# Optimization experiments

Hardware: AMD Instinct MI355X
Metric: run time of the kernel (lower is better)

## Reference

```python
import jax, jax.numpy as jnp
import numpy as np

N_NODES = 50000
D = 128
N_EDGES = 800000


def _gcn_layer(h, W, b, row, col, mask, n_nodes):
    # Linear: h @ W.T + b  (nn.Linear convention)
    h = h @ W.T + b
    # degree of source nodes, counting only non-self-loop edges (remove_self_loops)
    deg = jax.ops.segment_sum(mask.astype(h.dtype), row, num_segments=n_nodes)
    deg_inv_sqrt = jnp.where(deg > 0, jax.lax.rsqrt(jnp.maximum(deg, 1.0)), 0.0)
    norm = deg_inv_sqrt[row] * deg_inv_sqrt[col] * mask.astype(h.dtype)
    # gather-scale messages [E, D], scatter-add into target nodes (col)
    msg = norm[:, None] * h[row]
    return jax.ops.segment_sum(msg, col, num_segments=n_nodes)


def setup_inputs() -> dict:
    key = jax.random.key(0)
    ks = jax.random.split(key, 9)
    x = jax.random.normal(ks[0], (N_NODES, D), dtype=jnp.float32)
    edge_index = jax.random.randint(ks[1], (2, N_EDGES), 0, N_NODES, dtype=jnp.int64)
    lim = 1.0 / np.sqrt(D)
    params = {}
    for i in range(3):
        params[f"W{i}"] = jax.random.uniform(ks[2 + 2 * i], (D, D), jnp.float32, -lim, lim)
        params[f"b{i}"] = jax.random.uniform(ks[3 + 2 * i], (D,), jnp.float32, -lim, lim)
    return {"x": x, "edge_index": edge_index, **params}


def reference(x, edge_index, W0, b0, W1, b1, W2, b2):
    row, col = edge_index[0], edge_index[1]
    mask = row != col  # remove_self_loops
    h = x
    for W, b in ((W0, b0), (W1, b1), (W2, b2)):
        h_new = jax.nn.relu(_gcn_layer(h, W, b, row, col, mask, x.shape[0]))
        h = h + h_new
    return h
```

## Files before the change

### kernel.cpp

```cpp
#include <hip/hip_runtime.h>
#include <hip/hip_bf16.h>


#define D_DIM 128
#define SCAN_CHUNK 1024
#define CHUNKS 64
#define LDSW 12512

typedef __attribute__((ext_vector_type(8))) short bf16x8;
typedef __attribute__((ext_vector_type(4))) float f32x4;

static __device__ __forceinline__ short f2bf(float f) {
    union { __hip_bfloat16 b; short s; } u;
    u.b = __float2bfloat16(f);
    return u.s;
}
static __device__ __forceinline__ float bf_lo(unsigned p) { return __uint_as_float(p << 16); }
static __device__ __forceinline__ float bf_hi(unsigned p) { return __uint_as_float(p & 0xffff0000u); }


__global__ __launch_bounds__(256) void hist_kernel(const int* __restrict__ ei,
                                                   unsigned* __restrict__ partial_col,
                                                   unsigned* __restrict__ partial_row,
                                                   int E, int CHSZ) {
    __shared__ unsigned hh[LDSW];
    int tid = threadIdx.x;
    int ch = blockIdx.x;
    int docol = (blockIdx.y == 0);
    for (int i = tid; i < LDSW; i += 256) hh[i] = 0u;
    __syncthreads();
    int e0 = ch * CHSZ, e1 = min(e0 + CHSZ, E);
    for (int e = e0 + tid; e < e1; e += 256) {
        int row = ei[e];
        int col = ei[E + e];
        if (row == col) continue;
        int bin = docol ? col : row;
        atomicAdd(&hh[bin >> 2], 1u << ((bin & 3) * 8));
    }
    __syncthreads();
    unsigned* dst = (docol ? partial_col : partial_row) + ch * LDSW;
    for (int i = tid; i < LDSW; i += 256) dst[i] = hh[i];
}

__global__ __launch_bounds__(256) void reduce_scan_kernel(
    const unsigned* __restrict__ partial_col, const unsigned* __restrict__ partial_row,
    int* __restrict__ col_cnt, float* __restrict__ dis, int* __restrict__ bsum,
    int NW ) {
    __shared__ int wsum[4];
    int w = blockIdx.x * 256 + threadIdx.x;
    int s = 0;
    if (w < NW) {
        unsigned clo = 0, chi = 0, rlo = 0, rhi = 0;
#pragma unroll 4
        for (int ch = 0; ch < CHUNKS; ch++) {
            unsigned wc = partial_col[ch * LDSW + w];
            unsigned wr = partial_row[ch * LDSW + w];
            clo += wc & 0x00FF00FFu; chi += (wc >> 8) & 0x00FF00FFu;
            rlo += wr & 0x00FF00FFu; rhi += (wr >> 8) & 0x00FF00FFu;
        }
        int c0 = clo & 0xFFFF, c1 = chi & 0xFFFF, c2 = clo >> 16, c3 = chi >> 16;
        int r0 = rlo & 0xFFFF, r1 = rhi & 0xFFFF, r2 = rlo >> 16, r3 = rhi >> 16;
        ((int4*)col_cnt)[w] = make_int4(c0, c1, c2, c3);
        float4 dv;
        dv.x = (r0 > 0) ? rsqrtf((float)r0) : 0.0f;
        dv.y = (r1 > 0) ? rsqrtf((float)r1) : 0.0f;
        dv.z = (r2 > 0) ? rsqrtf((float)r2) : 0.0f;
        dv.w = (r3 > 0) ? rsqrtf((float)r3) : 0.0f;
        ((float4*)dis)[w] = dv;
        s = c0 + c1 + c2 + c3;
    }
#pragma unroll
    for (int d = 32; d > 0; d >>= 1) s += __shfl_down(s, d, 64);
    int lane = threadIdx.x & 63, wv = threadIdx.x >> 6;
    if (lane == 0) wsum[wv] = s;
    __syncthreads();
    if (threadIdx.x == 0) bsum[blockIdx.x] = wsum[0] + wsum[1] + wsum[2] + wsum[3];
}

__global__ __launch_bounds__(64) void scan_bbase_kernel(const int* __restrict__ bsum,
                                                        int* __restrict__ bbase,
                                                        int* __restrict__ offs,
                                                        int G, int n) {
    int lane = threadIdx.x;
    int v = (lane < G) ? bsum[lane] : 0;
    int s = v;
#pragma unroll
    for (int d = 1; d < 64; d <<= 1) {
        int t = __shfl_up(s, d, 64);
        if (lane >= d) s += t;
    }
    if (lane < G) bbase[lane] = s - v;
    if (lane == 63) offs[n] = s;
}

__global__ __launch_bounds__(256) void scan_final_kernel(const int* __restrict__ cnt,
                                                         const int* __restrict__ bbase,
                                                         int* __restrict__ offs, int n) {
    __shared__ int wsum[4];
    int base = blockIdx.x * SCAN_CHUNK;
    int tid = threadIdx.x;
    const int PT = SCAN_CHUNK / 256;
    int v[PT];
    int s = 0;
#pragma unroll
    for (int i = 0; i < PT; i++) {
        int g = base + tid * PT + i;
        v[i] = (g < n) ? cnt[g] : 0;
        s += v[i];
    }
    int local_sum = s;
    int lane = tid & 63, w = tid >> 6;
#pragma unroll
    for (int d = 1; d < 64; d <<= 1) {
        int t = __shfl_up(s, d, 64);
        if (lane >= d) s += t;
    }
    if (lane == 63) wsum[w] = s;
    __syncthreads();
    int wbase = 0;
    for (int i = 0; i < w; i++) wbase += wsum[i];
    int run = bbase[blockIdx.x] + wbase + (s - local_sum);
#pragma unroll
    for (int i = 0; i < PT; i++) {
        int g = base + tid * PT + i;
        if (g < n) offs[g] = run;
        run += v[i];
    }
}

__global__ __launch_bounds__(256) void base_kernel(const unsigned* __restrict__ partial_col,
                                                   const int* __restrict__ offs,
                                                   int* __restrict__ base,
                                                   int N, int NW) {
    int w = blockIdx.x * 256 + threadIdx.x;
    if (w >= NW) return;
    int4 run = ((const int4*)offs)[w];
    for (int ch = 0; ch < CHUNKS; ch++) {
        unsigned wd = partial_col[ch * LDSW + w];
        ((int4*)(base + ch * N))[w] = run;
        run.x += (int)(wd & 0xFF);
        run.y += (int)((wd >> 8) & 0xFF);
        run.z += (int)((wd >> 16) & 0xFF);
        run.w += (int)(wd >> 24);
    }
}

__global__ __launch_bounds__(256) void scatter_kernel(const int* __restrict__ ei,
                                                      const float* __restrict__ dis,
                                                      const int* __restrict__ base,
                                                      int2* __restrict__ epack,
                                                      int E, int N, int CHSZ) {
    __shared__ unsigned cur[LDSW];
    int tid = threadIdx.x;
    int ch = blockIdx.x;
    for (int i = tid; i < LDSW; i += 256) cur[i] = 0u;
    __syncthreads();
    int e0 = ch * CHSZ, e1 = min(e0 + CHSZ, E);
    const int* bch = base + ch * N;
    for (int e = e0 + tid; e < e1; e += 256) {
        int row = ei[e];
        int col = ei[E + e];
        if (row == col) continue;
        float w = dis[row] * dis[col];
        int sh = (col & 3) * 8;
        unsigned old = atomicAdd(&cur[col >> 2], 1u << sh);
        int slot = bch[col] + (int)((old >> sh) & 0xFF);
        epack[slot] = make_int2(row * (D_DIM / 2), __float_as_int(w));
    }
}

__global__ void wcvt_all_kernel(const float* __restrict__ W0, const float* __restrict__ W1,
                                const float* __restrict__ W2, unsigned short* __restrict__ B0,
                                unsigned short* __restrict__ B1, unsigned short* __restrict__ B2) {
    int i = blockIdx.x * blockDim.x + threadIdx.x;
    const float* W = (blockIdx.y == 0) ? W0 : (blockIdx.y == 1) ? W1 : W2;
    unsigned short* B = (blockIdx.y == 0) ? B0 : (blockIdx.y == 1) ? B1 : B2;
    if (i < D_DIM * D_DIM) B[i] = (unsigned short)f2bf(W[i]);
}


__global__ __launch_bounds__(256) void linear_mfma_kernel(
    const float* __restrict__ A, const unsigned short* __restrict__ Wb,
    const float* __restrict__ bias, unsigned short* __restrict__ hWb, int nrows) {
    int wave = threadIdx.x >> 6;
    int lane = threadIdx.x & 63;
    int r0 = blockIdx.x * 64 + wave * 16;
    int m = lane & 15, q = lane >> 4;
    int rload = min(r0 + m, nrows - 1);
    const float4* h4 = (const float4*)A;

    f32x4 acc[8];
#pragma unroll
    for (int jt = 0; jt < 8; jt++) acc[jt] = (f32x4){0.f, 0.f, 0.f, 0.f};

#pragma unroll
    for (int k0 = 0; k0 < 128; k0 += 32) {
        int c0 = k0 + q * 8;
        float4 x0 = h4[rload * 32 + (c0 >> 2)];
        float4 x1 = h4[rload * 32 + (c0 >> 2) + 1];
        bf16x8 a;
        a[0] = f2bf(x0.x); a[1] = f2bf(x0.y); a[2] = f2bf(x0.z); a[3] = f2bf(x0.w);
        a[4] = f2bf(x1.x); a[5] = f2bf(x1.y); a[6] = f2bf(x1.z); a[7] = f2bf(x1.w);
#pragma unroll
        for (int jt = 0; jt < 8; jt++) {
            bf16x8 b = *(const bf16x8*)(Wb + (jt * 16 + m) * D_DIM + c0);
            acc[jt] = __builtin_amdgcn_mfma_f32_16x16x32_bf16(a, b, acc[jt], 0, 0, 0);
        }
    }

#pragma unroll
    for (int jt = 0; jt < 8; jt++) {
        int col = jt * 16 + m;
        float bv = bias[col];
#pragma unroll
        for (int reg = 0; reg < 4; reg++) {
            int rr = r0 + q * 4 + reg;
            if (rr < nrows) hWb[(size_t)rr * D_DIM + col] = (unsigned short)f2bf(acc[jt][reg] + bv);
        }
    }
}

__global__ __launch_bounds__(256) void agg_kernel(const int* __restrict__ offs,
                                                  const int2* __restrict__ epack,
                                                  const unsigned int* __restrict__ hW2,
                                                  const float* __restrict__ hprev,
                                                  float* __restrict__ hout, int n_nodes) {
    int node = (int)((blockIdx.x * blockDim.x + threadIdx.x) >> 6);
    int lane = threadIdx.x & 63;
    if (node >= n_nodes) return;

    int beg = offs[node];
    int end = offs[node + 1];

    float ax8[8], ay8[8];
#pragma unroll
    for (int u = 0; u < 8; u++) { ax8[u] = 0.f; ay8[u] = 0.f; }

    int i = beg;
    for (; i + 8 <= end; i += 8) {
        int2 e[8];
        unsigned p[8];
#pragma unroll
        for (int u = 0; u < 8; u++) e[u] = epack[i + u];
#pragma unroll
        for (int u = 0; u < 8; u++) p[u] = hW2[e[u].x + lane];
#pragma unroll
        for (int u = 0; u < 8; u++) {
            float w = __int_as_float(e[u].y);
            ax8[u] = fmaf(w, bf_lo(p[u]), ax8[u]);
            ay8[u] = fmaf(w, bf_hi(p[u]), ay8[u]);
        }
    }
    int rem = end - i;
    if (rem & 4) {
        int2 e[4];
        unsigned p[4];
#pragma unroll
        for (int u = 0; u < 4; u++) e[u] = epack[i + u];
#pragma unroll
        for (int u = 0; u < 4; u++) p[u] = hW2[e[u].x + lane];
#pragma unroll
        for (int u = 0; u < 4; u++) {
            float w = __int_as_float(e[u].y);
            ax8[u] = fmaf(w, bf_lo(p[u]), ax8[u]);
            ay8[u] = fmaf(w, bf_hi(p[u]), ay8[u]);
        }
        i += 4;
    }
    if (rem & 2) {
        int2 e0 = epack[i], e1 = epack[i + 1];
        unsigned p0 = hW2[e0.x + lane], p1 = hW2[e1.x + lane];
        float w0 = __int_as_float(e0.y), w1 = __int_as_float(e1.y);
        ax8[4] = fmaf(w0, bf_lo(p0), ax8[4]); ay8[4] = fmaf(w0, bf_hi(p0), ay8[4]);
        ax8[5] = fmaf(w1, bf_lo(p1), ax8[5]); ay8[5] = fmaf(w1, bf_hi(p1), ay8[5]);
        i += 2;
    }
    if (rem & 1) {
        int2 e0 = epack[i];
        unsigned p0 = hW2[e0.x + lane];
        float w0 = __int_as_float(e0.y);
        ax8[6] = fmaf(w0, bf_lo(p0), ax8[6]); ay8[6] = fmaf(w0, bf_hi(p0), ay8[6]);
    }
    float ax = ((ax8[0] + ax8[1]) + (ax8[2] + ax8[3])) + ((ax8[4] + ax8[5]) + (ax8[6] + ax8[7]));
    float ay = ((ay8[0] + ay8[1]) + (ay8[2] + ay8[3])) + ((ay8[4] + ay8[5]) + (ay8[6] + ay8[7]));

    int idx = node * (D_DIM / 2) + lane;
    float2 hv = ((const float2*)hprev)[idx];
    float2 o;
    o.x = hv.x + fmaxf(ax, 0.0f);
    o.y = hv.y + fmaxf(ay, 0.0f);
    ((float2*)hout)[idx] = o;
}


static inline size_t align_up(size_t x, size_t a) { return (x + a - 1) & ~(a - 1); }

extern "C" void kernel_launch(void* const* d_in, const int* in_sizes, int n_in,
                              void* d_out, int out_size, void* d_ws, size_t ws_size,
                              hipStream_t stream) {
    const float* x = (const float*)d_in[0];
    const int* ei = (const int*)d_in[1];
    const float* Wl[3] = {(const float*)d_in[2], (const float*)d_in[4], (const float*)d_in[6]};
    const float* bl[3] = {(const float*)d_in[3], (const float*)d_in[5], (const float*)d_in[7]};

    const int N = in_sizes[0] / D_DIM;
    const int E = in_sizes[1] / 2;
    const int NW = N / 4;
    const int G = (N + SCAN_CHUNK - 1) / SCAN_CHUNK;
    const int CHSZ = (E + CHUNKS - 1) / CHUNKS;

    char* p = (char*)d_ws;
    int* col_cnt = (int*)p;            p += align_up((size_t)N * 4, 256);
    int* offs    = (int*)p;            p += align_up((size_t)(N + 1) * 4, 256);
    float* dis   = (float*)p;          p += align_up((size_t)N * 4, 256);
    int* bsum    = (int*)p;            p += align_up((size_t)64 * 4, 256);
    int* bbase   = (int*)p;            p += align_up((size_t)64 * 4, 256);
    unsigned* partial_col = (unsigned*)p;  p += align_up((size_t)CHUNKS * LDSW * 4, 256);
    unsigned* partial_row = (unsigned*)p;  p += align_up((size_t)CHUNKS * LDSW * 4, 256);
    int* base    = (int*)p;            p += align_up((size_t)CHUNKS * N * 4, 256);
    unsigned short* Wb[3];
    for (int l = 0; l < 3; l++) { Wb[l] = (unsigned short*)p; p += align_up((size_t)D_DIM * D_DIM * 2, 256); }
    int2* epack  = (int2*)p;           p += align_up((size_t)E * 8, 256);
    unsigned short* hWb = (unsigned short*)p;  p += align_up((size_t)N * D_DIM * 2, 256);
    (void)ws_size;

    hist_kernel<<<dim3(CHUNKS, 2), 256, 0, stream>>>(ei, partial_col, partial_row, E, CHSZ);
    reduce_scan_kernel<<<(NW + 255) / 256, 256, 0, stream>>>(partial_col, partial_row,
                                                             col_cnt, dis, bsum, NW);
    scan_bbase_kernel<<<1, 64, 0, stream>>>(bsum, bbase, offs, G, N);
    scan_final_kernel<<<G, 256, 0, stream>>>(col_cnt, bbase, offs, N);
    base_kernel<<<(NW + 255) / 256, 256, 0, stream>>>(partial_col, offs, base, N, NW);
    scatter_kernel<<<CHUNKS, 256, 0, stream>>>(ei, dis, base, epack, E, N, CHSZ);
    wcvt_all_kernel<<<dim3((D_DIM * D_DIM + 255) / 256, 3), 256, 0, stream>>>(
        Wl[0], Wl[1], Wl[2], Wb[0], Wb[1], Wb[2]);

    const float* hprev = x;
    float* h = (float*)d_out;
    int gemm_blocks = (N + 63) / 64;
    int agg_blocks = (N + 3) / 4;
    for (int l = 0; l < 3; l++) {
        linear_mfma_kernel<<<gemm_blocks, 256, 0, stream>>>(hprev, Wb[l], bl[l], hWb, N);
        agg_kernel<<<agg_blocks, 256, 0, stream>>>(offs, epack, (const unsigned int*)hWb, hprev, h, N);
        hprev = h;
    }
}
```

Baseline: 363.5 us.

## Quadruple edge chunks and replace per-chunk base array with grouped byte prefixes

```diff
diff --git a/kernel.cpp b/kernel.cpp
--- a/kernel.cpp
+++ b/kernel.cpp
@@ -4,7 +4,9 @@
 
 #define D_DIM 128
 #define SCAN_CHUNK 1024
-#define CHUNKS 64
+#define CHUNKS 256
+#define GROUPS 8
+#define GS (CHUNKS / GROUPS)
 #define LDSW 12512
 
 typedef __attribute__((ext_vector_type(8))) short bf16x8;
@@ -38,23 +40,46 @@
         atomicAdd(&hh[bin >> 2], 1u << ((bin & 3) * 8));
     }
     __syncthreads();
-    unsigned* dst = (docol ? partial_col : partial_row) + ch * LDSW;
+    unsigned* dst = (docol ? partial_col : partial_row) + (size_t)ch * LDSW;
     for (int i = tid; i < LDSW; i += 256) dst[i] = hh[i];
 }
 
-__global__ __launch_bounds__(256) void reduce_scan_kernel(
-    const unsigned* __restrict__ partial_col, const unsigned* __restrict__ partial_row,
-    int* __restrict__ col_cnt, float* __restrict__ dis, int* __restrict__ bsum,
-    int NW ) {
+__global__ __launch_bounds__(256) void group_prefix_kernel(
+    unsigned* __restrict__ partial_col, const unsigned* __restrict__ partial_row,
+    unsigned* __restrict__ gsum_col, unsigned* __restrict__ gsum_row, int NW) {
+    int w = blockIdx.x * 256 + threadIdx.x;
+    if (w >= NW) return;
+    int g = blockIdx.y;
+    size_t base = (size_t)(g * GS) * LDSW + w;
+    if (blockIdx.z == 0) {
+        unsigned run = 0;
+#pragma unroll 4
+        for (int c = 0; c < GS; c++) {
+            unsigned v = partial_col[base + (size_t)c * LDSW];
+            partial_col[base + (size_t)c * LDSW] = run;
+            run += v;
+        }
+        gsum_col[g * NW + w] = run;
+    } else {
+        unsigned run = 0;
+#pragma unroll 4
+        for (int c = 0; c < GS; c++) run += partial_row[base + (size_t)c * LDSW];
+        gsum_row[g * NW + w] = run;
+    }
+}
+
+__global__ __launch_bounds__(256) void cnt_dis_kernel(
+    const unsigned* __restrict__ gsum_col, const unsigned* __restrict__ gsum_row,
+    int* __restrict__ col_cnt, float* __restrict__ dis, int* __restrict__ bsum, int NW) {
     __shared__ int wsum[4];
     int w = blockIdx.x * 256 + threadIdx.x;
     int s = 0;
     if (w < NW) {
         unsigned clo = 0, chi = 0, rlo = 0, rhi = 0;
-#pragma unroll 4
-        for (int ch = 0; ch < CHUNKS; ch++) {
-            unsigned wc = partial_col[ch * LDSW + w];
-            unsigned wr = partial_row[ch * LDSW + w];
+#pragma unroll
+        for (int g = 0; g < GROUPS; g++) {
+            unsigned wc = gsum_col[g * NW + w];
+            unsigned wr = gsum_row[g * NW + w];
             clo += wc & 0x00FF00FFu; chi += (wc >> 8) & 0x00FF00FFu;
             rlo += wr & 0x00FF00FFu; rhi += (wr >> 8) & 0x00FF00FFu;
         }
@@ -128,44 +153,40 @@
     }
 }
 
-__global__ __launch_bounds__(256) void base_kernel(const unsigned* __restrict__ partial_col,
-                                                   const int* __restrict__ offs,
-                                                   int* __restrict__ base,
-                                                   int N, int NW) {
+__global__ __launch_bounds__(256) void group_base_kernel(
+    unsigned* __restrict__ partial_col, const unsigned* __restrict__ gsum_col, int NW) {
     int w = blockIdx.x * 256 + threadIdx.x;
     if (w >= NW) return;
-    int4 run = ((const int4*)offs)[w];
-    for (int ch = 0; ch < CHUNKS; ch++) {
-        unsigned wd = partial_col[ch * LDSW + w];
-        ((int4*)(base + ch * N))[w] = run;
-        run.x += (int)(wd & 0xFF);
-        run.y += (int)((wd >> 8) & 0xFF);
-        run.z += (int)((wd >> 16) & 0xFF);
-        run.w += (int)(wd >> 24);
-    }
+    int g = blockIdx.y + 1;
+    unsigned gb = 0;
+    for (int gp = 0; gp < g; gp++) gb += gsum_col[gp * NW + w];
+    size_t base = (size_t)(g * GS) * LDSW + w;
+#pragma unroll 4
+    for (int c = 0; c < GS; c++) partial_col[base + (size_t)c * LDSW] += gb;
 }
 
 __global__ __launch_bounds__(256) void scatter_kernel(const int* __restrict__ ei,
                                                       const float* __restrict__ dis,
-                                                      const int* __restrict__ base,
+                                                      const int* __restrict__ offs,
+                                                      const unsigned* __restrict__ chpref,
                                                       int2* __restrict__ epack,
-                                                      int E, int N, int CHSZ) {
+                                                      int E, int CHSZ) {
     __shared__ unsigned cur[LDSW];
     int tid = threadIdx.x;
     int ch = blockIdx.x;
     for (int i = tid; i < LDSW; i += 256) cur[i] = 0u;
     __syncthreads();
     int e0 = ch * CHSZ, e1 = min(e0 + CHSZ, E);
-    const int* bch = base + ch * N;
+    const unsigned* pf = chpref + (size_t)ch * LDSW;
     for (int e = e0 + tid; e < e1; e += 256) {
         int row = ei[e];
         int col = ei[E + e];
         if (row == col) continue;
-        float w = dis[row] * dis[col];
-        int sh = (col & 3) * 8;
-        unsigned old = atomicAdd(&cur[col >> 2], 1u << sh);
-        int slot = bch[col] + (int)((old >> sh) & 0xFF);
-        epack[slot] = make_int2(row * (D_DIM / 2), __float_as_int(w));
+        float wgt = dis[row] * dis[col];
+        int wd = col >> 2, sh = (col & 3) * 8;
+        unsigned old = atomicAdd(&cur[wd], 1u << sh);
+        int slot = offs[col] + (int)((pf[wd] >> sh) & 0xFFu) + (int)((old >> sh) & 0xFFu);
+        epack[slot] = make_int2(row * (D_DIM / 2), __float_as_int(wgt));
     }
 }
 
@@ -307,6 +328,7 @@
     const int E = in_sizes[1] / 2;
     const int NW = N / 4;
     const int G = (N + SCAN_CHUNK - 1) / SCAN_CHUNK;
+    const int NWB = (NW + 255) / 256;
     const int CHSZ = (E + CHUNKS - 1) / CHUNKS;
 
     char* p = (char*)d_ws;
@@ -317,7 +339,8 @@
     int* bbase   = (int*)p;            p += align_up((size_t)64 * 4, 256);
     unsigned* partial_col = (unsigned*)p;  p += align_up((size_t)CHUNKS * LDSW * 4, 256);
     unsigned* partial_row = (unsigned*)p;  p += align_up((size_t)CHUNKS * LDSW * 4, 256);
-    int* base    = (int*)p;            p += align_up((size_t)CHUNKS * N * 4, 256);
+    unsigned* gsum_col = (unsigned*)p; p += align_up((size_t)GROUPS * NW * 4, 256);
+    unsigned* gsum_row = (unsigned*)p; p += align_up((size_t)GROUPS * NW * 4, 256);
     unsigned short* Wb[3];
     for (int l = 0; l < 3; l++) { Wb[l] = (unsigned short*)p; p += align_up((size_t)D_DIM * D_DIM * 2, 256); }
     int2* epack  = (int2*)p;           p += align_up((size_t)E * 8, 256);
@@ -325,12 +348,13 @@
     (void)ws_size;
 
     hist_kernel<<<dim3(CHUNKS, 2), 256, 0, stream>>>(ei, partial_col, partial_row, E, CHSZ);
-    reduce_scan_kernel<<<(NW + 255) / 256, 256, 0, stream>>>(partial_col, partial_row,
-                                                             col_cnt, dis, bsum, NW);
+    group_prefix_kernel<<<dim3(NWB, GROUPS, 2), 256, 0, stream>>>(partial_col, partial_row,
+                                                                  gsum_col, gsum_row, NW);
+    cnt_dis_kernel<<<NWB, 256, 0, stream>>>(gsum_col, gsum_row, col_cnt, dis, bsum, NW);
     scan_bbase_kernel<<<1, 64, 0, stream>>>(bsum, bbase, offs, G, N);
     scan_final_kernel<<<G, 256, 0, stream>>>(col_cnt, bbase, offs, N);
-    base_kernel<<<(NW + 255) / 256, 256, 0, stream>>>(partial_col, offs, base, N, NW);
-    scatter_kernel<<<CHUNKS, 256, 0, stream>>>(ei, dis, base, epack, E, N, CHSZ);
+    group_base_kernel<<<dim3(NWB, GROUPS - 1), 256, 0, stream>>>(partial_col, gsum_col, NW);
+    scatter_kernel<<<CHUNKS, 256, 0, stream>>>(ei, dis, offs, partial_col, epack, E, CHSZ);
     wcvt_all_kernel<<<dim3((D_DIM * D_DIM + 255) / 256, 3), 256, 0, stream>>>(
         Wl[0], Wl[1], Wl[2], Wb[0], Wb[1], Wb[2]);
 
```

Measured after the change: 326.4 us. -10.2%, faster.
